# Optimization experiments

Measured on AMD Instinct MI355X. Metric: run time of the kernel, lower is better.

## Reference

```python
import jax, jax.numpy as jnp
import numpy as np
import math

D_MODEL = 1024
NUM_HEADS = 16


def setup_inputs() -> dict:
    key = jax.random.key(0)
    ks = jax.random.split(key, 5)
    B, S, D = 4, 2048, D_MODEL
    scale = 1.0 / math.sqrt(D)
    x = jax.random.normal(ks[0], (B, S, D), dtype=jnp.float32)
    wq = jax.random.normal(ks[1], (D, D), dtype=jnp.float32) * scale
    wk = jax.random.normal(ks[2], (D, D), dtype=jnp.float32) * scale
    wv = jax.random.normal(ks[3], (D, D), dtype=jnp.float32) * scale
    wo = jax.random.normal(ks[4], (D, D), dtype=jnp.float32) * scale
    return {"x": x, "wq": wq, "wk": wk, "wv": wv, "wo": wo}


def _mhsa(x, wq, wk, wv, wo):
    B, S, D = x.shape
    H = NUM_HEADS
    dk = D // H
    # projections: y = x @ W^T
    q = (x @ wq.T).reshape(B, S, H, dk).transpose(0, 2, 1, 3)  # [B,H,S,dk]
    k = (x @ wk.T).reshape(B, S, H, dk).transpose(0, 2, 1, 3)
    v = (x @ wv.T).reshape(B, S, H, dk).transpose(0, 2, 1, 3)
    scores = jnp.einsum("bhqd,bhkd->bhqk", q, k) / jnp.sqrt(jnp.asarray(dk, x.dtype))
    mask = jnp.tril(jnp.ones((S, S), dtype=bool))  # [S,S] causal
    neg_inf = jnp.asarray(-jnp.inf, scores.dtype)
    scores_masked = jnp.where(mask, scores, neg_inf)
    max_scores = jnp.max(scores_masked, axis=-1, keepdims=True)
    max_scores = jnp.where(jnp.isfinite(max_scores), max_scores, jnp.zeros_like(max_scores))
    exp_scores = jnp.exp(scores - max_scores) * mask.astype(scores.dtype)
    denom = jnp.maximum(exp_scores.sum(axis=-1, keepdims=True), 1e-9)
    attn = exp_scores / denom
    out = jnp.einsum("bhqk,bhkd->bhqd", attn, v)  # [B,H,S,dk]
    out = out.transpose(0, 2, 1, 3).reshape(B, S, D)
    return out @ wo.T


def reference(x, wq, wk, wv, wo):
    return _mhsa(x, wq, wk, wv, wo)
```

## Files before the change

kernel.cpp:

```cpp
#include <hip/hip_runtime.h>
#include <stdint.h>


typedef __attribute__((ext_vector_type(8))) short short8;
typedef __attribute__((ext_vector_type(4))) short short4v;
typedef __attribute__((ext_vector_type(4))) float float4v;
typedef __attribute__((ext_vector_type(2))) unsigned int uint2v;

#define QSCALE 0.18033688011112042f
#define EXP_C2 5.770780163555852f

__device__ inline short f2bf(float f) {
  union { float f; uint32_t u; } v; v.f = f;
  uint32_t r = (v.u + 0x7fffu + ((v.u >> 16) & 1)) >> 16;
  return (short)(uint16_t)r;
}

__device__ inline unsigned int pack2bf(float a, float b) {
  union { float f; unsigned int u; } ua, ub;
  ua.f = a; ub.f = b;
  return __builtin_amdgcn_perm(ub.u, ua.u, 0x07060302u);
}

__device__ inline void async_copy16(const void* g, void* l) {
  __builtin_amdgcn_global_load_lds(
      (const __attribute__((address_space(1))) void*)g,
      (__attribute__((address_space(3))) void*)l, 16, 0, 0);
}

__global__ __launch_bounds__(256) void cvtAll(
    const float* __restrict__ x, const float* __restrict__ wq,
    const float* __restrict__ wk, const float* __restrict__ wv,
    const float* __restrict__ wo,
    short* __restrict__ xb, short* __restrict__ wqb, short* __restrict__ wkb,
    short* __restrict__ wvb, short* __restrict__ wob) {
  const int b = blockIdx.x;
  const float* s; short* d; int base;
  if (b < 8192) { s = x; d = xb; base = b; }
  else {
    const int wi = (b - 8192) >> 10; base = (b - 8192) & 1023;
    s = (wi == 0) ? wq : (wi == 1) ? wk : (wi == 2) ? wv : wo;
    d = (wi == 0) ? wqb : (wi == 1) ? wkb : (wi == 2) ? wvb : wob;
  }
  const size_t i = (size_t)base * 256 + threadIdx.x;
  const float4v v = *(const float4v*)(s + 4 * i);
  short4v o;
  o[0] = f2bf(v[0]); o[1] = f2bf(v[1]);
  o[2] = f2bf(v[2]); o[3] = f2bf(v[3]);
  *(short4v*)(d + 4 * i) = o;
}

template <int MODE>
__global__ __launch_bounds__(256) void gemm_bt(
    const short* __restrict__ A,
    const short* __restrict__ W0, const short* __restrict__ W1,
    short* __restrict__ Yb0, short* __restrict__ Yb1,
    float* __restrict__ Yf) {
  constexpr int Kd = 1024;
  __shared__ __align__(16) short As[128 * 32];
  __shared__ __align__(16) short Bs[128 * 32];

  const int t = threadIdx.x;
  const int w = t >> 6, l = t & 63, l15 = l & 15, quad = l >> 4;
  const int wm = w >> 1, wn = w & 1;

  int mblk, nblk, zz = 0;
  {
    const int o = blockIdx.x;
    const int xcd = o & 7, slot = o >> 3;
    mblk = (xcd << 3) | (slot & 7);
    const int c = slot >> 3;
    if (MODE == 0) { nblk = c & 7; zz = c >> 3; }
    else nblk = c;
  }
  const int m0 = mblk * 128, n0 = nblk * 128;

  const short* W = W0;
  short* Yb = Yb0;
  float sc = 1.0f;
  if (MODE == 0) {
    if (zz == 0) sc = QSCALE;
    else { W = W1; Yb = Yb1; }
  }

  float4v acc[4][4];
#pragma unroll
  for (int i = 0; i < 4; i++)
#pragma unroll
    for (int j = 0; j < 4; j++) acc[i][j] = (float4v){0.f, 0.f, 0.f, 0.f};

  const int r4 = t >> 2, c48 = (t & 3) * 8;
  const short* Wbase = W + (n0 + r4) * Kd + c48;
  short* AsW = &As[w * 512];
  short* BsW = &Bs[w * 512];
  const int i0 = m0 + r4;
  const int i1 = m0 + 64 + r4;

  for (int k0 = 0; k0 < Kd; k0 += 32) {
    if (MODE != 1) {
      async_copy16(A + (size_t)i0 * Kd + k0 + c48, AsW);
      async_copy16(A + (size_t)i1 * Kd + k0 + c48, AsW + 2048);
    } else {
      const int k = k0 + c48, h = k >> 6, dd = k & 63;
      async_copy16(A + ((((size_t)(i0 >> 11) * 16 + h) * 2048 + (i0 & 2047)) * 64 + dd), AsW);
      async_copy16(A + ((((size_t)(i1 >> 11) * 16 + h) * 2048 + (i1 & 2047)) * 64 + dd), AsW + 2048);
    }
    async_copy16(Wbase + k0, BsW);
    async_copy16(Wbase + 64 * Kd + k0, BsW + 2048);
    __syncthreads();
    short8 af[4], bf[4];
#pragma unroll
    for (int mi = 0; mi < 4; mi++)
      af[mi] = *(const short8*)&As[(wm * 64 + mi * 16 + l15) * 32 + quad * 8];
#pragma unroll
    for (int ni = 0; ni < 4; ni++)
      bf[ni] = *(const short8*)&Bs[(wn * 64 + ni * 16 + l15) * 32 + quad * 8];
#pragma unroll
    for (int mi = 0; mi < 4; mi++)
#pragma unroll
      for (int ni = 0; ni < 4; ni++)
        acc[mi][ni] = __builtin_amdgcn_mfma_f32_16x16x32_bf16(
            af[mi], bf[ni], acc[mi][ni], 0, 0, 0);
    __syncthreads();
  }

#pragma unroll
  for (int mi = 0; mi < 4; mi++) {
    const int ib = m0 + wm * 64 + mi * 16 + quad * 4;
#pragma unroll
    for (int ni = 0; ni < 4; ni++) {
      const int j = n0 + wn * 64 + ni * 16 + l15;
      if (MODE == 2) {
        short4v o;
#pragma unroll
        for (int r = 0; r < 4; r++) o[r] = f2bf(acc[mi][ni][r]);
        *(short4v*)&Yb[(((size_t)(ib >> 11) * 16 + (j >> 6)) * 64 + (j & 63)) * 2048 +
                       (ib & 2047)] = o;
      } else {
#pragma unroll
        for (int r = 0; r < 4; r++) {
          const int i = ib + r;
          if (MODE == 0) {
            Yb[((((size_t)(i >> 11) * 16 + (j >> 6)) * 2048 + (i & 2047)) * 64 + (j & 63))] =
                f2bf(acc[mi][ni][r] * sc);
          } else {
            Yf[(size_t)i * 1024 + j] = acc[mi][ni][r];
          }
        }
      }
    }
  }
}

__global__ __launch_bounds__(256) void attn4(
    short* __restrict__ Q,
    const short* __restrict__ K,
    const short* __restrict__ VT) {
  __shared__ __align__(16) short Ks[2][64 * 64];
  __shared__ __align__(16) short Vs[2][64 * 64];
  __shared__ __align__(16) short Ps[4][16 * 64];

  const int t = threadIdx.x;
  const int w = t >> 6, l = t & 63, l15 = l & 15, quad = l >> 4;
  const int bh = blockIdx.x;
  const int qp = blockIdx.y;
  short* Qh = Q + (size_t)bh * 2048 * 64;
  const short* Kh = K + (size_t)bh * 2048 * 64;
  const short* Vh = VT + (size_t)bh * 64 * 2048;

  const int sr = t >> 2, c0 = t & 3;
  const int ssw = sr & 7;
  const int stA = sr * 64 + (((2 * c0) ^ ssw) << 3);
  const int stB = sr * 64 + (((2 * c0 + 1) ^ ssw) << 3);
  const int gA = c0 * 16, gB = c0 * 16 + 8;

  const int fsw = l15 & 7;
  const int fc0 = (quad ^ fsw) << 3;
  const int fc1 = ((4 + quad) ^ fsw) << 3;
  short* PsW = &Ps[w][0];
  const int pwr = l15 * 64;

  short8 ones;
#pragma unroll
  for (int j = 0; j < 8; j++) ones[j] = (short)0x3F80;
  const float4v initC = (float4v){-EXP_C2, -EXP_C2, -EXP_C2, -EXP_C2};

  for (int pass = 0; pass < 2; pass++) {
    const int q0 = (pass ? (31 - qp) : qp) * 64;
    const int qn = q0 + w * 16 + l15;
    const short8 qf0 = *(const short8*)&Qh[(size_t)qn * 64 + quad * 8];
    const short8 qf1 = *(const short8*)&Qh[(size_t)qn * 64 + 32 + quad * 8];

    float4v acc[4];
#pragma unroll
    for (int dt = 0; dt < 4; dt++) acc[dt] = (float4v){0.f, 0.f, 0.f, 0.f};
    float4v accL = (float4v){0.f, 0.f, 0.f, 0.f};

    short8 kv0 = *(const short8*)&Kh[(size_t)sr * 64 + gA];
    short8 kv1 = *(const short8*)&Kh[(size_t)sr * 64 + gB];
    short8 vv0 = *(const short8*)&Vh[(size_t)sr * 2048 + gA];
    short8 vv1 = *(const short8*)&Vh[(size_t)sr * 2048 + gB];

    int p = 0;
    for (int kb = 0; kb <= q0; kb += 64, p ^= 1) {
      const bool diag = (kb == q0);
      short* KsP = &Ks[p][0];
      short* VsP = &Vs[p][0];
      *(short8*)&KsP[stA] = kv0;
      *(short8*)&KsP[stB] = kv1;
      *(short8*)&VsP[stA] = vv0;
      *(short8*)&VsP[stB] = vv1;
      __syncthreads();

      const int kb2 = diag ? kb : kb + 64;
      kv0 = *(const short8*)&Kh[(size_t)(kb2 + sr) * 64 + gA];
      kv1 = *(const short8*)&Kh[(size_t)(kb2 + sr) * 64 + gB];
      vv0 = *(const short8*)&Vh[(size_t)sr * 2048 + kb2 + gA];
      vv1 = *(const short8*)&Vh[(size_t)sr * 2048 + kb2 + gB];

#pragma unroll
      for (int kt = 0; kt < 4; kt++) {
        const int krb = (kt * 16 + l15) * 64;
        const short8 kf0 = *(const short8*)&KsP[krb + fc0];
        const short8 kf1 = *(const short8*)&KsP[krb + fc1];
        __builtin_amdgcn_s_setprio(1);
        float4v s = __builtin_amdgcn_mfma_f32_16x16x32_bf16(kf0, qf0, initC, 0, 0, 0);
        s = __builtin_amdgcn_mfma_f32_16x16x32_bf16(kf1, qf1, s, 0, 0, 0);
        __builtin_amdgcn_s_setprio(0);
        float p0 = __builtin_amdgcn_exp2f(s[0]);
        float p1 = __builtin_amdgcn_exp2f(s[1]);
        float p2 = __builtin_amdgcn_exp2f(s[2]);
        float p3 = __builtin_amdgcn_exp2f(s[3]);
        if (diag) {
          const int key = kb + kt * 16 + quad * 4;
          p0 = (key <= qn) ? p0 : 0.f;
          p1 = (key + 1 <= qn) ? p1 : 0.f;
          p2 = (key + 2 <= qn) ? p2 : 0.f;
          p3 = (key + 3 <= qn) ? p3 : 0.f;
        }
        uint2v pw;
        pw[0] = pack2bf(p0, p1);
        pw[1] = pack2bf(p2, p3);
        *(uint2v*)&PsW[pwr + (((2 * kt + (quad >> 1)) ^ fsw) << 3) +
                       ((quad & 1) << 2)] = pw;
      }
      __builtin_amdgcn_wave_barrier();

      const short8 pf0 = *(const short8*)&PsW[pwr + fc0];
      const short8 pf1 = *(const short8*)&PsW[pwr + fc1];
      __builtin_amdgcn_s_setprio(1);
#pragma unroll
      for (int dt = 0; dt < 4; dt++) {
        const int vrb = (dt * 16 + l15) * 64;
        const short8 vf0 = *(const short8*)&VsP[vrb + fc0];
        const short8 vf1 = *(const short8*)&VsP[vrb + fc1];
        acc[dt] = __builtin_amdgcn_mfma_f32_16x16x32_bf16(vf0, pf0, acc[dt], 0, 0, 0);
        acc[dt] = __builtin_amdgcn_mfma_f32_16x16x32_bf16(vf1, pf1, acc[dt], 0, 0, 0);
      }
      accL = __builtin_amdgcn_mfma_f32_16x16x32_bf16(ones, pf0, accL, 0, 0, 0);
      accL = __builtin_amdgcn_mfma_f32_16x16x32_bf16(ones, pf1, accL, 0, 0, 0);
      __builtin_amdgcn_s_setprio(0);
    }

    const float inv = 1.0f / fmaxf(accL[0], 1e-30f);
#pragma unroll
    for (int dt = 0; dt < 4; dt++) {
      short4v o;
#pragma unroll
      for (int ri = 0; ri < 4; ri++) o[ri] = f2bf(acc[dt][ri] * inv);
      *(short4v*)&Qh[(size_t)qn * 64 + dt * 16 + quad * 4] = o;
    }
    if (pass == 0) __syncthreads();
  }
}

extern "C" void kernel_launch(void* const* d_in, const int* in_sizes, int n_in,
                              void* d_out, int out_size, void* d_ws,
                              size_t ws_size, hipStream_t stream) {
  const float* x = (const float*)d_in[0];
  const float* wq = (const float*)d_in[1];
  const float* wk = (const float*)d_in[2];
  const float* wv = (const float*)d_in[3];
  const float* wo = (const float*)d_in[4];
  float* out = (float*)d_out;

  short* xb = (short*)d_out;
  short* vtg = xb + (size_t)8192 * 1024;

  short* wqb = (short*)d_ws;
  short* wkb = wqb + (size_t)1024 * 1024;
  short* wvb = wkb + (size_t)1024 * 1024;
  short* wob = wvb + (size_t)1024 * 1024;
  short* qws = wob + (size_t)1024 * 1024;
  short* kws = qws + (size_t)8192 * 1024;

  cvtAll<<<12288, 256, 0, stream>>>(x, wq, wk, wv, wo, xb, wqb, wkb, wvb, wob);
  gemm_bt<0><<<1024, 256, 0, stream>>>(
      xb, wqb, wkb, qws, kws, nullptr);
  gemm_bt<2><<<512, 256, 0, stream>>>(
      xb, wvb, nullptr, vtg, nullptr, nullptr);
  attn4<<<dim3(64, 16), 256, 0, stream>>>(qws, kws, vtg);
  gemm_bt<1><<<512, 256, 0, stream>>>(
      qws, wob, nullptr, nullptr, nullptr, out);
}
```

Before: 252.2 us.

## Stage K/V tiles with async global-to-LDS copies instead of register staging

Replaces the register-staged K/V double-buffering (global load into registers, then ds_write) with direct asynchronous global-to-LDS copies into the alternate buffer. The swizzle moves from the LDS write side to the global read addresses, so each lane writes a contiguous 16-byte slot. This is meant to drop the LDS store instructions and the staging registers, which could raise occupancy and overlap better. The risk is correctness if the wait on outstanding copies before the barrier is missing or misplaced.

```diff
diff --git a/kernel.cpp b/kernel.cpp
--- a/kernel.cpp
+++ b/kernel.cpp
@@ -168,11 +168,11 @@
   const short* Kh = K + (size_t)bh * 2048 * 64;
   const short* Vh = VT + (size_t)bh * 64 * 2048;
 
-  const int sr = t >> 2, c0 = t & 3;
-  const int ssw = sr & 7;
-  const int stA = sr * 64 + (((2 * c0) ^ ssw) << 3);
-  const int stB = sr * 64 + (((2 * c0 + 1) ^ ssw) << 3);
-  const int gA = c0 * 16, gB = c0 * 16 + 8;
+  const int r0 = t >> 3;
+  const int jsw = ((t & 7) ^ (r0 & 7)) << 3;
+  const int koff = r0 * 64 + jsw;
+  const int voff = r0 * 2048 + jsw;
+  const int ldsW = w * 512;
 
   const int fsw = l15 & 7;
   const int fc0 = (quad ^ fsw) << 3;
@@ -196,27 +196,26 @@
     for (int dt = 0; dt < 4; dt++) acc[dt] = (float4v){0.f, 0.f, 0.f, 0.f};
     float4v accL = (float4v){0.f, 0.f, 0.f, 0.f};
 
-    short8 kv0 = *(const short8*)&Kh[(size_t)sr * 64 + gA];
-    short8 kv1 = *(const short8*)&Kh[(size_t)sr * 64 + gB];
-    short8 vv0 = *(const short8*)&Vh[(size_t)sr * 2048 + gA];
-    short8 vv1 = *(const short8*)&Vh[(size_t)sr * 2048 + gB];
+    async_copy16(Kh + koff, &Ks[0][ldsW]);
+    async_copy16(Kh + 2048 + koff, &Ks[0][2048 + ldsW]);
+    async_copy16(Vh + voff, &Vs[0][ldsW]);
+    async_copy16(Vh + 65536 + voff, &Vs[0][2048 + ldsW]);
 
     int p = 0;
     for (int kb = 0; kb <= q0; kb += 64, p ^= 1) {
       const bool diag = (kb == q0);
-      short* KsP = &Ks[p][0];
-      short* VsP = &Vs[p][0];
-      *(short8*)&KsP[stA] = kv0;
-      *(short8*)&KsP[stB] = kv1;
-      *(short8*)&VsP[stA] = vv0;
-      *(short8*)&VsP[stB] = vv1;
       __syncthreads();
 
-      const int kb2 = diag ? kb : kb + 64;
-      kv0 = *(const short8*)&Kh[(size_t)(kb2 + sr) * 64 + gA];
-      kv1 = *(const short8*)&Kh[(size_t)(kb2 + sr) * 64 + gB];
-      vv0 = *(const short8*)&Vh[(size_t)sr * 2048 + kb2 + gA];
-      vv1 = *(const short8*)&Vh[(size_t)sr * 2048 + kb2 + gB];
+      if (!diag) {
+        const int kb2 = kb + 64;
+        const size_t kB = (size_t)kb2 * 64;
+        async_copy16(Kh + kB + koff, &Ks[p ^ 1][ldsW]);
+        async_copy16(Kh + kB + 2048 + koff, &Ks[p ^ 1][2048 + ldsW]);
+        async_copy16(Vh + kb2 + voff, &Vs[p ^ 1][ldsW]);
+        async_copy16(Vh + kb2 + 65536 + voff, &Vs[p ^ 1][2048 + ldsW]);
+      }
+      const short* KsP = &Ks[p][0];
+      const short* VsP = &Vs[p][0];
 
 #pragma unroll
       for (int kt = 0; kt < 4; kt++) {
```

After: 256.4 us. No clear change (+1.7%).
